# Kernel tuning notes

Measured on AMD Instinct MI355X. Metric: run time of the kernel, lower is better.

Reference implementation:

```python
import jax, jax.numpy as jnp
import numpy as np

N, D = 131072, 64
VOCAB = 1_000_000
N_NEG = 1024
TEMPERATURE = 1.0
EPS = 1e-10
NEG_FILL = -1e9


def setup_inputs() -> dict:
    key = jax.random.key(0)
    k1, k2, k3, k4, k5 = jax.random.split(key, 5)
    hidden = jax.random.normal(k1, (N, D), dtype=jnp.float32)
    y = jax.random.randint(k2, (N,), 0, VOCAB, dtype=jnp.int64)
    sampled_indices = jax.random.randint(k3, (N_NEG,), 0, VOCAB, dtype=jnp.int64)
    emb_table = jax.random.normal(k4, (VOCAB, D), dtype=jnp.float32) * 0.02
    p = jax.random.uniform(k5, (VOCAB,), dtype=jnp.float32) + EPS
    sampling_probs = p / p.sum()  # normalized popularity distribution (buffer)
    return {"hidden": hidden, "y": y, "sampled_indices": sampled_indices,
            "emb_table": emb_table, "sampling_probs": sampling_probs}


def reference(hidden, y, sampled_indices, emb_table, sampling_probs):
    # torch masks rows with y == 0 before the loss; we use weighted mean instead
    # (identical math, jit-friendly static shapes).
    mask = (y != 0).astype(hidden.dtype)                      # [N]
    e_pos = emb_table[y]                                      # [N, D] gather
    e_neg = emb_table[sampled_indices]                        # [K, D] gather
    pos_logits = jnp.einsum('nd,nd->n', hidden, e_pos)        # [N]
    neg_logits = hidden @ e_neg.T                             # [N, K]
    collision = y[:, None] == sampled_indices[None, :]        # [N, K]
    neg_logits = jnp.where(collision, NEG_FILL, neg_logits)
    true_probs = sampling_probs[y]                            # [N]
    sample_probs = sampling_probs[sampled_indices]            # [K]
    pos = pos_logits / TEMPERATURE - jnp.log(true_probs + EPS)        # [N]
    neg = neg_logits / TEMPERATURE - jnp.log(sample_probs + EPS)[None, :]
    logits = jnp.concatenate([pos[:, None], neg], axis=1)     # [N, 1+K]
    # cross-entropy with label 0: logsumexp - logits[:, 0]
    ce = jax.nn.logsumexp(logits, axis=-1) - logits[:, 0]     # [N]
    return jnp.sum(ce * mask) / jnp.maximum(jnp.sum(mask), 1.0)
```

## Files before the change

kernel.cpp:

```cpp
#include <hip/hip_runtime.h>

#define N_ROWS 131072
#define DIM 64
#define KNEG 1024
#define FEPS 1e-10f
#define LOG2E 1.4426950408889634f
#define HSLOTS 2048
#define CPI 64
#define OUTER (KNEG / CPI)
#define CSTR 72

typedef __attribute__((ext_vector_type(8))) short bf16x8;
typedef __attribute__((ext_vector_type(4))) float f32x4;

__device__ __forceinline__ unsigned short f2bf(float x) {
    unsigned int u = __float_as_uint(x);
    unsigned int r = (u + 0x7fffu + ((u >> 16) & 1u)) >> 16;
    return (unsigned short)r;
}

#if __has_builtin(__builtin_amdgcn_exp2f)
__device__ __forceinline__ float fexp2(float x) { return __builtin_amdgcn_exp2f(x); }
#else
__device__ __forceinline__ float fexp2(float x) {
    float r; asm("v_exp_f32 %0, %1\ns_nop 1" : "=v"(r) : "v"(x)); return r;
}
#endif

__device__ __forceinline__ bf16x8 cvt8(float4 u, float4 v) {
    bf16x8 r;
    r[0] = (short)f2bf(u.x * LOG2E); r[1] = (short)f2bf(u.y * LOG2E);
    r[2] = (short)f2bf(u.z * LOG2E); r[3] = (short)f2bf(u.w * LOG2E);
    r[4] = (short)f2bf(v.x * LOG2E); r[5] = (short)f2bf(v.y * LOG2E);
    r[6] = (short)f2bf(v.z * LOG2E); r[7] = (short)f2bf(v.w * LOG2E);
    return r;
}

__global__ __launch_bounds__(256) void prep_k(
    const float* __restrict__ emb, const int* __restrict__ sidx,
    const float* __restrict__ probs,
    unsigned short* __restrict__ enegPK, float* __restrict__ lf,
    float* __restrict__ gv, int* __restrict__ hkey, float* __restrict__ hval)
{
    const int tid = threadIdx.x;
    if (blockIdx.x < 64) {
        const int gid = blockIdx.x * 256 + tid;
        const int col = gid >> 4;
        const int j   = gid & 15;
        const int c = sidx[col];
        const float4 v = *(const float4*)(emb + (size_t)c * DIM + j * 4);
        unsigned int lo = (unsigned int)f2bf(v.x) | ((unsigned int)f2bf(v.y) << 16);
        unsigned int hi = (unsigned int)f2bf(v.z) | ((unsigned int)f2bf(v.w) << 16);
        ((uint2*)enegPK)[(size_t)col * 16 + j] = make_uint2(lo, hi);
    } else {
        for (int s = tid; s < HSLOTS; s += 256) { hkey[s] = -1; hval[s] = 0.0f; }
        float L[4];
        float m = -1e30f;
        int cs[4];
#pragma unroll
        for (int i = 0; i < 4; ++i) {
            cs[i] = sidx[tid * 4 + i];
            L[i] = logf(probs[cs[i]] + FEPS);
            m = fmaxf(m, -L[i]);
        }
        __shared__ float red[256];
        red[tid] = m;
        __syncthreads();
        for (int s2 = 128; s2 > 0; s2 >>= 1) {
            if (tid < s2) red[tid] = fmaxf(red[tid], red[tid + s2]);
            __syncthreads();
        }
        const float G = red[0] + 2.0f;
        if (tid == 0) gv[0] = G;
#pragma unroll
        for (int i = 0; i < 4; ++i) {
            const float lfv = (-L[i] - G) * LOG2E;
            lf[tid * 4 + i] = lfv;
            const float fc = exp2f(lfv);
            unsigned int slot = ((unsigned int)cs[i] * 2654435761u) & (HSLOTS - 1);
            for (int it = 0; it < HSLOTS; ++it) {
                int old = atomicCAS(&hkey[slot], -1, cs[i]);
                if (old == -1 || old == cs[i]) { atomicAdd(&hval[slot], fc); break; }
                slot = (slot + 1) & (HSLOTS - 1);
            }
        }
    }
}

__global__ __launch_bounds__(256, 4) void main_k(
    const float* __restrict__ hidden, const int* __restrict__ y,
    const float* __restrict__ emb, const float* __restrict__ probs,
    const unsigned short* __restrict__ enegPK, const float* __restrict__ lf,
    const float* __restrict__ gv, const int* __restrict__ hkey,
    const float* __restrict__ hval,
    float* __restrict__ pv, float* __restrict__ pw)
{
    __shared__ __align__(16) short bt[2][CPI * CSTR];
    __shared__ float lf_lds[KNEG];

    const int tid  = threadIdx.x;
    const int wid  = tid >> 6;
    const int lane = tid & 63;
    const int quad = lane >> 4;
    const int l15  = lane & 15;

    const int row0 = (blockIdx.x * 4 + wid) * 32;
    const int r0 = row0 + l15;
    const int r1 = r0 + 16;

    const int y0 = y[r0];
    const int y1 = y[r1];

    for (int i = tid; i < KNEG; i += 256) lf_lds[i] = lf[i];

    const uint4* g4 = (const uint4*)enegPK;
    const int cw0 = tid >> 3;
    const int cw1 = (tid + 256) >> 3;
    const int ow  = tid & 7;
    {
        uint4 u0 = g4[tid], u1 = g4[tid + 256];
        *((uint4*)(&bt[0][cw0 * CSTR]) + ow) = u0;
        *((uint4*)(&bt[0][cw1 * CSTR]) + ow) = u1;
    }

    const float* hp0 = hidden + (size_t)r0 * DIM + quad * 8;
    const float* hp1 = hidden + (size_t)r1 * DIM + quad * 8;
    const float4 a0 = *(const float4*)(hp0 + 0);
    const float4 a1 = *(const float4*)(hp0 + 4);
    const float4 a2 = *(const float4*)(hp0 + 32);
    const float4 a3 = *(const float4*)(hp0 + 36);
    const float4 c0 = *(const float4*)(hp1 + 0);
    const float4 c1 = *(const float4*)(hp1 + 4);
    const float4 c2 = *(const float4*)(hp1 + 32);
    const float4 c3 = *(const float4*)(hp1 + 36);

    const float* pe0 = emb + (size_t)y0 * DIM + quad * 8;
    const float* pe1 = emb + (size_t)y1 * DIM + quad * 8;
    const float4 e0 = *(const float4*)(pe0 + 0);
    const float4 e1 = *(const float4*)(pe0 + 4);
    const float4 e2 = *(const float4*)(pe0 + 32);
    const float4 e3 = *(const float4*)(pe0 + 36);
    const float4 g0 = *(const float4*)(pe1 + 0);
    const float4 g1 = *(const float4*)(pe1 + 4);
    const float4 g2 = *(const float4*)(pe1 + 32);
    const float4 g3 = *(const float4*)(pe1 + 36);
    float pd0 = a0.x*e0.x + a0.y*e0.y + a0.z*e0.z + a0.w*e0.w
              + a1.x*e1.x + a1.y*e1.y + a1.z*e1.z + a1.w*e1.w
              + a2.x*e2.x + a2.y*e2.y + a2.z*e2.z + a2.w*e2.w
              + a3.x*e3.x + a3.y*e3.y + a3.z*e3.z + a3.w*e3.w;
    float pd1 = c0.x*g0.x + c0.y*g0.y + c0.z*g0.z + c0.w*g0.w
              + c1.x*g1.x + c1.y*g1.y + c1.z*g1.z + c1.w*g1.w
              + c2.x*g2.x + c2.y*g2.y + c2.z*g2.z + c2.w*g2.w
              + c3.x*g3.x + c3.y*g3.y + c3.z*g3.z + c3.w*g3.w;
    pd0 += __shfl_xor(pd0, 16, 64); pd0 += __shfl_xor(pd0, 32, 64);
    pd1 += __shfl_xor(pd1, 16, 64); pd1 += __shfl_xor(pd1, 32, 64);

    const bf16x8 h00 = cvt8(a0, a1), h01 = cvt8(a2, a3);
    const bf16x8 h10 = cvt8(c0, c1), h11 = cvt8(c2, c3);

    __syncthreads();

    float s00 = 0.f, s01 = 0.f, s02 = 0.f, s03 = 0.f;
    float s10 = 0.f, s11 = 0.f, s12 = 0.f, s13 = 0.f;
    int p = 0;

    for (int t = 0; t < OUTER; ++t) {
        uint4 u0, u1;
        const bool has = (t + 1 < OUTER);
        if (has) {
            const uint4* gs = g4 + (t + 1) * 512;
            u0 = gs[tid]; u1 = gs[tid + 256];
        }
#pragma unroll
        for (int tt = 0; tt < CPI / 16; ++tt) {
            const short* bp = &bt[p][(tt * 16 + l15) * CSTR + quad * 8];
            const bf16x8 b0 = *(const bf16x8*)bp;
            const bf16x8 b1 = *(const bf16x8*)(bp + 32);
            const float lfv = lf_lds[t * CPI + tt * 16 + l15];
            f32x4 acc0 = {lfv, lfv, lfv, lfv};
            acc0 = __builtin_amdgcn_mfma_f32_16x16x32_bf16(h00, b0, acc0, 0, 0, 0);
            acc0 = __builtin_amdgcn_mfma_f32_16x16x32_bf16(h01, b1, acc0, 0, 0, 0);
            f32x4 acc1 = {lfv, lfv, lfv, lfv};
            acc1 = __builtin_amdgcn_mfma_f32_16x16x32_bf16(h10, b0, acc1, 0, 0, 0);
            acc1 = __builtin_amdgcn_mfma_f32_16x16x32_bf16(h11, b1, acc1, 0, 0, 0);
            s00 += fexp2(acc0[0]); s01 += fexp2(acc0[1]);
            s02 += fexp2(acc0[2]); s03 += fexp2(acc0[3]);
            s10 += fexp2(acc1[0]); s11 += fexp2(acc1[1]);
            s12 += fexp2(acc1[2]); s13 += fexp2(acc1[3]);
        }
        if (has) {
            *((uint4*)(&bt[p ^ 1][cw0 * CSTR]) + ow) = u0;
            *((uint4*)(&bt[p ^ 1][cw1 * CSTR]) + ow) = u1;
        }
        __syncthreads();
        p ^= 1;
    }

#pragma unroll
    for (int m = 8; m > 0; m >>= 1) {
        s00 += __shfl_xor(s00, m, 64); s01 += __shfl_xor(s01, m, 64);
        s02 += __shfl_xor(s02, m, 64); s03 += __shfl_xor(s03, m, 64);
        s10 += __shfl_xor(s10, m, 64); s11 += __shfl_xor(s11, m, 64);
        s12 += __shfl_xor(s12, m, 64); s13 += __shfl_xor(s13, m, 64);
    }
    float sa0 = (lane & 1) ? s01 : s00;
    float sb0 = (lane & 1) ? s03 : s02;
    float sv0 = (lane & 2) ? sb0 : sa0;
    sv0 = __shfl(sv0, ((l15 >> 2) << 4) + l15, 64);
    float sa1 = (lane & 1) ? s11 : s10;
    float sb1 = (lane & 1) ? s13 : s12;
    float sv1 = (lane & 2) ? sb1 : sa1;
    sv1 = __shfl(sv1, ((l15 >> 2) << 4) + l15, 64);

    const float G = gv[0];
    float v = 0.f, ww = 0.f;
    {
        const float pos = pd0 - logf(probs[y0] + FEPS);
        float H = 0.0f;
        unsigned int slot = ((unsigned int)y0 * 2654435761u) & (HSLOTS - 1);
        for (int it = 0; it < HSLOTS; ++it) {
            const int k = hkey[slot];
            if (k == y0) { H = hval[slot]; break; }
            if (k == -1) break;
            slot = (slot + 1) & (HSLOTS - 1);
        }
        float sneg = fmaxf(sv0 - exp2f(pd0 * LOG2E) * H, 0.0f);
        const float M = fmaxf(G, pos);
        const float lse = M + logf(exp2f((pos - M) * LOG2E) + sneg * exp2f((G - M) * LOG2E));
        const float w = (y0 != 0) ? 1.0f : 0.0f;
        v += (lse - pos) * w; ww += w;
    }
    {
        const float pos = pd1 - logf(probs[y1] + FEPS);
        float H = 0.0f;
        unsigned int slot = ((unsigned int)y1 * 2654435761u) & (HSLOTS - 1);
        for (int it = 0; it < HSLOTS; ++it) {
            const int k = hkey[slot];
            if (k == y1) { H = hval[slot]; break; }
            if (k == -1) break;
            slot = (slot + 1) & (HSLOTS - 1);
        }
        float sneg = fmaxf(sv1 - exp2f(pd1 * LOG2E) * H, 0.0f);
        const float M = fmaxf(G, pos);
        const float lse = M + logf(exp2f((pos - M) * LOG2E) + sneg * exp2f((G - M) * LOG2E));
        const float w = (y1 != 0) ? 1.0f : 0.0f;
        v += (lse - pos) * w; ww += w;
    }
#pragma unroll
    for (int m = 8; m > 0; m >>= 1) {
        v  += __shfl_xor(v, m, 64);
        ww += __shfl_xor(ww, m, 64);
    }
    if (lane == 0) {
        const int wgid = blockIdx.x * 4 + wid;
        pv[wgid] = v;
        pw[wgid] = ww;
    }
}

__global__ __launch_bounds__(256) void fin_k(
    const float* __restrict__ pv, const float* __restrict__ pw,
    float* __restrict__ out)
{
    const int tid = threadIdx.x;
    double av = 0.0, aw = 0.0;
    for (int i = tid; i < N_ROWS / 32; i += 256) { av += pv[i]; aw += pw[i]; }
    __shared__ double rv[256], rw[256];
    rv[tid] = av; rw[tid] = aw;
    __syncthreads();
    for (int s2 = 128; s2 > 0; s2 >>= 1) {
        if (tid < s2) { rv[tid] += rv[tid + s2]; rw[tid] += rw[tid + s2]; }
        __syncthreads();
    }
    if (tid == 0) {
        double c = rw[0] < 1.0 ? 1.0 : rw[0];
        out[0] = (float)(rv[0] / c);
    }
}

extern "C" void kernel_launch(void* const* d_in, const int* in_sizes, int n_in,
                              void* d_out, int out_size, void* d_ws, size_t ws_size,
                              hipStream_t stream) {
    const float* hidden = (const float*)d_in[0];
    const int*   yv     = (const int*)d_in[1];
    const int*   sidx   = (const int*)d_in[2];
    const float* emb    = (const float*)d_in[3];
    const float* probs  = (const float*)d_in[4];
    float* out = (float*)d_out;

    char* ws = (char*)d_ws;
    unsigned short* enegPK = (unsigned short*)(ws);
    float* lf   = (float*)(ws + 131072);
    float* gv   = (float*)(ws + 135168);
    int*   hkey = (int*)(ws + 135424);
    float* hval = (float*)(ws + 143616);
    float* pv   = (float*)(ws + 151808);
    float* pw   = (float*)(ws + 168192);

    prep_k<<<65, 256, 0, stream>>>(emb, sidx, probs, enegPK, lf, gv, hkey, hval);
    main_k<<<N_ROWS / 128, 256, 0, stream>>>(hidden, yv, emb, probs, enegPK,
                                             lf, gv, hkey, hval, pv, pw);
    fin_k<<<1, 256, 0, stream>>>(pv, pw, out);
}
```

Before: 64.19 us.

## Process 64 rows per wave to reuse each LDS negative tile across four MFMA row blocks

Each wave now handles four 16-row blocks instead of two, so every bf16 negative-embedding fragment read from LDS feeds four MFMA pairs. This halves the block count and the per-row cost of LDS reads, global staging and barriers. All gathers, including the probs lookup, are issued up front to overlap their latency. Launch bounds drop to 2 blocks per CU to leave room for the larger register footprint, which lowers occupancy; the s_nop after the inline v_exp fallback is also removed.

Measured after the change: 77.75 us. 21.1% more time.

```diff
diff --git a/kernel.cpp b/kernel.cpp
--- a/kernel.cpp
+++ b/kernel.cpp
@@ -9,6 +9,7 @@
 #define CPI 64
 #define OUTER (KNEG / CPI)
 #define CSTR 72
+#define RPW 64
 
 typedef __attribute__((ext_vector_type(8))) short bf16x8;
 typedef __attribute__((ext_vector_type(4))) float f32x4;
@@ -23,7 +24,7 @@
 __device__ __forceinline__ float fexp2(float x) { return __builtin_amdgcn_exp2f(x); }
 #else
 __device__ __forceinline__ float fexp2(float x) {
-    float r; asm("v_exp_f32 %0, %1\ns_nop 1" : "=v"(r) : "v"(x)); return r;
+    float r; asm("v_exp_f32 %0, %1" : "=v"(r) : "v"(x)); return r;
 }
 #endif
 
@@ -87,7 +88,7 @@
     }
 }
 
-__global__ __launch_bounds__(256, 4) void main_k(
+__global__ __launch_bounds__(256, 2) void main_k(
     const float* __restrict__ hidden, const int* __restrict__ y,
     const float* __restrict__ emb, const float* __restrict__ probs,
     const unsigned short* __restrict__ enegPK, const float* __restrict__ lf,
@@ -104,12 +105,32 @@
     const int quad = lane >> 4;
     const int l15  = lane & 15;
 
-    const int row0 = (blockIdx.x * 4 + wid) * 32;
-    const int r0 = row0 + l15;
-    const int r1 = r0 + 16;
-
-    const int y0 = y[r0];
-    const int y1 = y[r1];
+    const int row0 = (blockIdx.x * 4 + wid) * RPW;
+
+    int yy[4];
+#pragma unroll
+    for (int p2 = 0; p2 < 4; ++p2) yy[p2] = y[row0 + p2 * 16 + l15];
+
+    float4 hf[4][4];
+#pragma unroll
+    for (int p2 = 0; p2 < 4; ++p2) {
+        const float* hp = hidden + (size_t)(row0 + p2 * 16 + l15) * DIM + quad * 8;
+        hf[p2][0] = *(const float4*)(hp + 0);
+        hf[p2][1] = *(const float4*)(hp + 4);
+        hf[p2][2] = *(const float4*)(hp + 32);
+        hf[p2][3] = *(const float4*)(hp + 36);
+    }
+    float4 ef[4][4];
+    float qy[4];
+#pragma unroll
+    for (int p2 = 0; p2 < 4; ++p2) {
+        const float* pe = emb + (size_t)yy[p2] * DIM + quad * 8;
+        ef[p2][0] = *(const float4*)(pe + 0);
+        ef[p2][1] = *(const float4*)(pe + 4);
+        ef[p2][2] = *(const float4*)(pe + 32);
+        ef[p2][3] = *(const float4*)(pe + 36);
+        qy[p2] = probs[yy[p2]];
+    }
 
     for (int i = tid; i < KNEG; i += 256) lf_lds[i] = lf[i];
 
@@ -123,47 +144,34 @@
         *((uint4*)(&bt[0][cw1 * CSTR]) + ow) = u1;
     }
 
-    const float* hp0 = hidden + (size_t)r0 * DIM + quad * 8;
-    const float* hp1 = hidden + (size_t)r1 * DIM + quad * 8;
-    const float4 a0 = *(const float4*)(hp0 + 0);
-    const float4 a1 = *(const float4*)(hp0 + 4);
-    const float4 a2 = *(const float4*)(hp0 + 32);
-    const float4 a3 = *(const float4*)(hp0 + 36);
-    const float4 c0 = *(const float4*)(hp1 + 0);
-    const float4 c1 = *(const float4*)(hp1 + 4);
-    const float4 c2 = *(const float4*)(hp1 + 32);
-    const float4 c3 = *(const float4*)(hp1 + 36);
-
-    const float* pe0 = emb + (size_t)y0 * DIM + quad * 8;
-    const float* pe1 = emb + (size_t)y1 * DIM + quad * 8;
-    const float4 e0 = *(const float4*)(pe0 + 0);
-    const float4 e1 = *(const float4*)(pe0 + 4);
-    const float4 e2 = *(const float4*)(pe0 + 32);
-    const float4 e3 = *(const float4*)(pe0 + 36);
-    const float4 g0 = *(const float4*)(pe1 + 0);
-    const float4 g1 = *(const float4*)(pe1 + 4);
-    const float4 g2 = *(const float4*)(pe1 + 32);
-    const float4 g3 = *(const float4*)(pe1 + 36);
-    float pd0 = a0.x*e0.x + a0.y*e0.y + a0.z*e0.z + a0.w*e0.w
-              + a1.x*e1.x + a1.y*e1.y + a1.z*e1.z + a1.w*e1.w
-              + a2.x*e2.x + a2.y*e2.y + a2.z*e2.z + a2.w*e2.w
-              + a3.x*e3.x + a3.y*e3.y + a3.z*e3.z + a3.w*e3.w;
-    float pd1 = c0.x*g0.x + c0.y*g0.y + c0.z*g0.z + c0.w*g0.w
-              + c1.x*g1.x + c1.y*g1.y + c1.z*g1.z + c1.w*g1.w
-              + c2.x*g2.x + c2.y*g2.y + c2.z*g2.z + c2.w*g2.w
-              + c3.x*g3.x + c3.y*g3.y + c3.z*g3.z + c3.w*g3.w;
-    pd0 += __shfl_xor(pd0, 16, 64); pd0 += __shfl_xor(pd0, 32, 64);
-    pd1 += __shfl_xor(pd1, 16, 64); pd1 += __shfl_xor(pd1, 32, 64);
-
-    const bf16x8 h00 = cvt8(a0, a1), h01 = cvt8(a2, a3);
-    const bf16x8 h10 = cvt8(c0, c1), h11 = cvt8(c2, c3);
+    float pd[4];
+    bf16x8 hb[4][2];
+#pragma unroll
+    for (int p2 = 0; p2 < 4; ++p2) {
+        float d = hf[p2][0].x*ef[p2][0].x + hf[p2][0].y*ef[p2][0].y
+                + hf[p2][0].z*ef[p2][0].z + hf[p2][0].w*ef[p2][0].w
+                + hf[p2][1].x*ef[p2][1].x + hf[p2][1].y*ef[p2][1].y
+                + hf[p2][1].z*ef[p2][1].z + hf[p2][1].w*ef[p2][1].w
+                + hf[p2][2].x*ef[p2][2].x + hf[p2][2].y*ef[p2][2].y
+                + hf[p2][2].z*ef[p2][2].z + hf[p2][2].w*ef[p2][2].w
+                + hf[p2][3].x*ef[p2][3].x + hf[p2][3].y*ef[p2][3].y
+                + hf[p2][3].z*ef[p2][3].z + hf[p2][3].w*ef[p2][3].w;
+        d += __shfl_xor(d, 16, 64);
+        d += __shfl_xor(d, 32, 64);
+        pd[p2] = d;
+        hb[p2][0] = cvt8(hf[p2][0], hf[p2][1]);
+        hb[p2][1] = cvt8(hf[p2][2], hf[p2][3]);
+    }
 
     __syncthreads();
 
-    float s00 = 0.f, s01 = 0.f, s02 = 0.f, s03 = 0.f;
-    float s10 = 0.f, s11 = 0.f, s12 = 0.f, s13 = 0.f;
-    int p = 0;
-
+    float sac[4][4];
+#pragma unroll
+    for (int p2 = 0; p2 < 4; ++p2)
+#pragma unroll
+        for (int e = 0; e < 4; ++e) sac[p2][e] = 0.0f;
+
+    int pb = 0;
     for (int t = 0; t < OUTER; ++t) {
         uint4 u0, u1;
         const bool has = (t + 1 < OUTER);
@@ -173,77 +181,61 @@
         }
 #pragma unroll
         for (int tt = 0; tt < CPI / 16; ++tt) {
-            const short* bp = &bt[p][(tt * 16 + l15) * CSTR + quad * 8];
+            const short* bp = &bt[pb][(tt * 16 + l15) * CSTR + quad * 8];
             const bf16x8 b0 = *(const bf16x8*)bp;
             const bf16x8 b1 = *(const bf16x8*)(bp + 32);
             const float lfv = lf_lds[t * CPI + tt * 16 + l15];
-            f32x4 acc0 = {lfv, lfv, lfv, lfv};
-            acc0 = __builtin_amdgcn_mfma_f32_16x16x32_bf16(h00, b0, acc0, 0, 0, 0);
-            acc0 = __builtin_amdgcn_mfma_f32_16x16x32_bf16(h01, b1, acc0, 0, 0, 0);
-            f32x4 acc1 = {lfv, lfv, lfv, lfv};
-            acc1 = __builtin_amdgcn_mfma_f32_16x16x32_bf16(h10, b0, acc1, 0, 0, 0);
-            acc1 = __builtin_amdgcn_mfma_f32_16x16x32_bf16(h11, b1, acc1, 0, 0, 0);
-            s00 += fexp2(acc0[0]); s01 += fexp2(acc0[1]);
-            s02 += fexp2(acc0[2]); s03 += fexp2(acc0[3]);
-            s10 += fexp2(acc1[0]); s11 += fexp2(acc1[1]);
-            s12 += fexp2(acc1[2]); s13 += fexp2(acc1[3]);
+#pragma unroll
+            for (int p2 = 0; p2 < 4; ++p2) {
+                f32x4 acc = {lfv, lfv, lfv, lfv};
+                acc = __builtin_amdgcn_mfma_f32_16x16x32_bf16(hb[p2][0], b0, acc, 0, 0, 0);
+                acc = __builtin_amdgcn_mfma_f32_16x16x32_bf16(hb[p2][1], b1, acc, 0, 0, 0);
+                sac[p2][0] += fexp2(acc[0]);
+                sac[p2][1] += fexp2(acc[1]);
+                sac[p2][2] += fexp2(acc[2]);
+                sac[p2][3] += fexp2(acc[3]);
+            }
         }
         if (has) {
-            *((uint4*)(&bt[p ^ 1][cw0 * CSTR]) + ow) = u0;
-            *((uint4*)(&bt[p ^ 1][cw1 * CSTR]) + ow) = u1;
+            *((uint4*)(&bt[pb ^ 1][cw0 * CSTR]) + ow) = u0;
+            *((uint4*)(&bt[pb ^ 1][cw1 * CSTR]) + ow) = u1;
         }
         __syncthreads();
-        p ^= 1;
-    }
-
-#pragma unroll
-    for (int m = 8; m > 0; m >>= 1) {
-        s00 += __shfl_xor(s00, m, 64); s01 += __shfl_xor(s01, m, 64);
-        s02 += __shfl_xor(s02, m, 64); s03 += __shfl_xor(s03, m, 64);
-        s10 += __shfl_xor(s10, m, 64); s11 += __shfl_xor(s11, m, 64);
-        s12 += __shfl_xor(s12, m, 64); s13 += __shfl_xor(s13, m, 64);
-    }
-    float sa0 = (lane & 1) ? s01 : s00;
-    float sb0 = (lane & 1) ? s03 : s02;
-    float sv0 = (lane & 2) ? sb0 : sa0;
-    sv0 = __shfl(sv0, ((l15 >> 2) << 4) + l15, 64);
-    float sa1 = (lane & 1) ? s11 : s10;
-    float sb1 = (lane & 1) ? s13 : s12;
-    float sv1 = (lane & 2) ? sb1 : sa1;
-    sv1 = __shfl(sv1, ((l15 >> 2) << 4) + l15, 64);
+        pb ^= 1;
+    }
+
+#pragma unroll
+    for (int p2 = 0; p2 < 4; ++p2)
+#pragma unroll
+        for (int e = 0; e < 4; ++e) {
+#pragma unroll
+            for (int m = 8; m > 0; m >>= 1)
+                sac[p2][e] += __shfl_xor(sac[p2][e], m, 64);
+        }
 
     const float G = gv[0];
     float v = 0.f, ww = 0.f;
-    {
-        const float pos = pd0 - logf(probs[y0] + FEPS);
+#pragma unroll
+    for (int p2 = 0; p2 < 4; ++p2) {
+        float sa = (lane & 1) ? sac[p2][1] : sac[p2][0];
+        float sb = (lane & 1) ? sac[p2][3] : sac[p2][2];
+        float sv = (lane & 2) ? sb : sa;
+        sv = __shfl(sv, ((l15 >> 2) << 4) + l15, 64);
+
+        const int yv = yy[p2];
+        const float pos = pd[p2] - logf(qy[p2] + FEPS);
         float H = 0.0f;
-        unsigned int slot = ((unsigned int)y0 * 2654435761u) & (HSLOTS - 1);
+        unsigned int slot = ((unsigned int)yv * 2654435761u) & (HSLOTS - 1);
         for (int it = 0; it < HSLOTS; ++it) {
             const int k = hkey[slot];
-            if (k == y0) { H = hval[slot]; break; }
+            if (k == yv) { H = hval[slot]; break; }
             if (k == -1) break;
             slot = (slot + 1) & (HSLOTS - 1);
         }
-        float sneg = fmaxf(sv0 - exp2f(pd0 * LOG2E) * H, 0.0f);
+        float sneg = fmaxf(sv - exp2f(pd[p2] * LOG2E) * H, 0.0f);
         const float M = fmaxf(G, pos);
         const float lse = M + logf(exp2f((pos - M) * LOG2E) + sneg * exp2f((G - M) * LOG2E));
-        const float w = (y0 != 0) ? 1.0f : 0.0f;
-        v += (lse - pos) * w; ww += w;
-    }
-    {
-        const float pos = pd1 - logf(probs[y1] + FEPS);
-        float H = 0.0f;
-        unsigned int slot = ((unsigned int)y1 * 2654435761u) & (HSLOTS - 1);
-        for (int it = 0; it < HSLOTS; ++it) {
-            const int k = hkey[slot];
-            if (k == y1) { H = hval[slot]; break; }
-            if (k == -1) break;
-            slot = (slot + 1) & (HSLOTS - 1);
-        }
-        float sneg = fmaxf(sv1 - exp2f(pd1 * LOG2E) * H, 0.0f);
-        const float M = fmaxf(G, pos);
-        const float lse = M + logf(exp2f((pos - M) * LOG2E) + sneg * exp2f((G - M) * LOG2E));
-        const float w = (y1 != 0) ? 1.0f : 0.0f;
+        const float w = (yv != 0) ? 1.0f : 0.0f;
         v += (lse - pos) * w; ww += w;
     }
 #pragma unroll
@@ -264,7 +256,7 @@
 {
     const int tid = threadIdx.x;
     double av = 0.0, aw = 0.0;
-    for (int i = tid; i < N_ROWS / 32; i += 256) { av += pv[i]; aw += pw[i]; }
+    for (int i = tid; i < N_ROWS / RPW; i += 256) { av += pv[i]; aw += pw[i]; }
     __shared__ double rv[256], rw[256];
     rv[tid] = av; rw[tid] = aw;
     __syncthreads();
@@ -298,7 +290,7 @@
     float* pw   = (float*)(ws + 168192);
 
     prep_k<<<65, 256, 0, stream>>>(emb, sidx, probs, enegPK, lf, gv, hkey, hval);
-    main_k<<<N_ROWS / 128, 256, 0, stream>>>(hidden, yv, emb, probs, enegPK,
-                                             lf, gv, hkey, hval, pv, pw);
+    main_k<<<N_ROWS / (4 * RPW), 256, 0, stream>>>(hidden, yv, emb, probs, enegPK,
+                                                   lf, gv, hkey, hval, pv, pw);
     fin_k<<<1, 256, 0, stream>>>(pv, pw, out);
 }
```
